# Performance work log

Measured on AMD Instinct MI355X. Metric: run time of the kernel, lower is better.

The kernel has to match this reference:

```python
import jax, jax.numpy as jnp
import numpy as np

K = 3  # conv1d kernel size
PAD = (K - 1) // 2


def _conv1d_1ch(x, w, b):
    # x: (B, 1, C), w: (1, 1, K), b: (1,)  -- torch Conv1d cross-correlation
    c = x.shape[-1]
    xp = jnp.pad(x, ((0, 0), (0, 0), (PAD, PAD)))
    y = sum(w[0, 0, k] * xp[:, :, k:k + c] for k in range(K))
    return y + b[0]


def setup_inputs() -> dict:
    key = jax.random.key(0)
    ks = jax.random.split(key, 13)
    B, C, H, W, E = 8, 256, 48, 48, 64
    s = lambda fan: 1.0 / np.sqrt(fan)
    return {
        "feature": jax.random.normal(ks[0], (B, C, H, W), jnp.float32),
        "wq1": jax.random.normal(ks[1], (1, 1, K), jnp.float32) * s(K),
        "bq1": jax.random.normal(ks[2], (1,), jnp.float32) * s(K),
        "wk1": jax.random.normal(ks[3], (1, 1, K), jnp.float32) * s(K),
        "bk1": jax.random.normal(ks[4], (1,), jnp.float32) * s(K),
        "wq2": jax.random.normal(ks[5], (E, C), jnp.float32) * s(C),
        "bq2": jax.random.normal(ks[6], (E,), jnp.float32) * s(C),
        "wk2": jax.random.normal(ks[7], (E, C), jnp.float32) * s(C),
        "bk2": jax.random.normal(ks[8], (E,), jnp.float32) * s(C),
        "wv2": jax.random.normal(ks[9], (E, C), jnp.float32) * s(C),
        "bv2": jax.random.normal(ks[10], (E,), jnp.float32) * s(C),
        "watt": jax.random.normal(ks[11], (C, E), jnp.float32) * s(E),
        "batt": jax.random.normal(ks[12], (C,), jnp.float32) * s(E),
    }


def reference(feature, wq1, bq1, wk1, bk1, wq2, bq2, wk2, bk2, wv2, bv2, watt, batt):
    b, c, h, w = feature.shape
    hw = h * w

    # ---- Global Channel Attention ----
    gap = jnp.mean(feature, axis=(2, 3)).reshape(b, 1, c)
    query = jax.nn.sigmoid(_conv1d_1ch(gap, wq1, bq1))  # (b,1,c)
    key_ = jax.nn.sigmoid(_conv1d_1ch(gap, wk1, bk1))   # (b,1,c)
    att_c = key_[:, 0, :, None] * query[:, 0, None, :]  # (b,c,c) = K^T Q
    att_c = jax.nn.softmax(att_c, axis=1)               # softmax over dim=1
    value = feature.reshape(b, hw, c)                   # raw reshape, as in torch
    gc = jnp.matmul(value, att_c).reshape(b, c, h, w)   # raw reshape back

    # ---- Global Spatial Attention ----
    q = (jnp.einsum('bchw,ec->behw', feature, wq2) + bq2[None, :, None, None]).reshape(b, -1, hw)
    k = (jnp.einsum('bchw,ec->behw', feature, wk2) + bk2[None, :, None, None]).reshape(b, -1, hw)
    v = (jnp.einsum('bchw,ec->behw', feature, wv2) + bv2[None, :, None, None]).reshape(b, -1, hw)
    att_s = jnp.einsum('bei,bej->bij', k, q)            # (b,hw,hw)
    att_s = jax.nn.softmax(att_s, axis=2)
    gs = jnp.einsum('bei,bij->bej', v, att_s).reshape(b, -1, h, w)  # (b,e,h,w)
    gs = jnp.einsum('behw,ce->bchw', gs, watt) + batt[None, :, None, None]

    # ---- Gated combination ----
    feature_gc = feature * gc
    return feature_gc * gs + feature_gc
```

## Files before the change

kernel.cpp:

```cpp
#include <hip/hip_runtime.h>

#define B_ 8
#define C_ 256
#define HW_ 2304
#define E_ 64
#define SB_ (C_*HW_)
#define LOG2E_ 1.44269504088896340736f

typedef unsigned short u16;
typedef __attribute__((ext_vector_type(8))) __bf16 bf16x8;
typedef __attribute__((ext_vector_type(4))) float f32x4;
#define MFMA16(a,b,c) __builtin_amdgcn_mfma_f32_16x16x32_bf16(a,b,c,0,0,0)

#define LDS_FENCE() do { asm volatile("s_waitcnt lgkmcnt(0)" ::: "memory"); \
                         __builtin_amdgcn_sched_barrier(0); } while(0)

static __device__ inline u16 f2bf(float x){
  unsigned u = __builtin_bit_cast(unsigned, x);
  u += 0x7FFFu + ((u >> 16) & 1u);
  return (u16)(u >> 16);
}
static __device__ inline float bf2f(u16 h){
  unsigned u = ((unsigned)h) << 16;
  return __builtin_bit_cast(float, u);
}


struct KFrag { bf16x8 h0, h1, l0, l1; };
static __device__ __forceinline__ KFrag ldfrag(const u16* __restrict__ ph,
                                               const u16* __restrict__ pl,
                                               size_t tile, int lane){
  KFrag q;
  q.h0 = *(const bf16x8*)(ph + (tile*2+0)*512 + (size_t)lane*8);
  q.h1 = *(const bf16x8*)(ph + (tile*2+1)*512 + (size_t)lane*8);
  q.l0 = *(const bf16x8*)(pl + (tile*2+0)*512 + (size_t)lane*8);
  q.l1 = *(const bf16x8*)(pl + (tile*2+1)*512 + (size_t)lane*8);
  return q;
}

__global__ __launch_bounds__(256) void k_gap(const float* __restrict__ f, float* __restrict__ gap){
  int bc = blockIdx.x;
  const float* row = f + (size_t)bc * HW_;
  float s = 0.f;
  for (int i = threadIdx.x; i < HW_; i += 256) s += row[i];
  #pragma unroll
  for (int off = 32; off; off >>= 1) s += __shfl_down(s, off);
  __shared__ float red[4];
  int lane = threadIdx.x & 63, wv = threadIdx.x >> 6;
  if (lane == 0) red[wv] = s;
  __syncthreads();
  if (threadIdx.x == 0) gap[bc] = (red[0]+red[1]+red[2]+red[3]) * (1.0f/HW_);
}

__global__ __launch_bounds__(256) void k_attc2(const float* __restrict__ gap,
    const float* __restrict__ wq1, const float* __restrict__ bq1,
    const float* __restrict__ wk1, const float* __restrict__ bk1,
    u16* __restrict__ ath, u16* __restrict__ atl){
  int b = blockIdx.x >> 8;
  int j = blockIdx.x & 255;
  int i = threadIdx.x;
  const float* g = gap + b*C_;
  float gm1 = (i > 0)      ? g[i-1] : 0.f;
  float g0  = g[i];
  float gp1 = (i < C_-1)   ? g[i+1] : 0.f;
  float keyv = wk1[0]*gm1 + wk1[1]*g0 + wk1[2]*gp1 + bk1[0];
  keyv = 1.f/(1.f+__expf(-keyv));
  float qm1 = (j > 0)      ? g[j-1] : 0.f;
  float q0  = g[j];
  float qp1 = (j < C_-1)   ? g[j+1] : 0.f;
  float qv = wq1[0]*qm1 + wq1[1]*q0 + wq1[2]*qp1 + bq1[0];
  qv = 1.f/(1.f+__expf(-qv));
  float s = keyv * qv;
  __shared__ float red[256];
  red[i] = s; __syncthreads();
  for (int st = 128; st > 0; st >>= 1){ if (i < st) red[i] = fmaxf(red[i], red[i+st]); __syncthreads(); }
  float mx = red[0]; __syncthreads();
  float e = __expf(s - mx);
  red[i] = e; __syncthreads();
  for (int st = 128; st > 0; st >>= 1){ if (i < st) red[i] += red[i+st]; __syncthreads(); }
  float sum = red[0];
  float x = e / sum;
  u16 hb = f2bf(x);
  size_t o = (((size_t)b*16 + (j>>4))*8 + (i>>5))*512 + (((i&31)>>3)*16 + (j&15))*8 + (i&7);
  ath[o] = hb;
  atl[o] = f2bf(x - bf2f(hb));
}

__global__ __launch_bounds__(256) void k_wcvt(const float* __restrict__ wq,
    const float* __restrict__ wk, const float* __restrict__ wv,
    u16* __restrict__ wbh, u16* __restrict__ wbl){
  int n = blockIdx.x*256 + threadIdx.x;
  int mz = n >> 14; int idx = n & 16383;
  int e = idx >> 8, c = idx & 255;
  const float* w = (mz==0) ? wq : ((mz==1) ? wk : wv);
  float x = w[idx] * ((mz==1) ? LOG2E_ : 1.0f);
  u16 hb = f2bf(x);
  size_t widx = (((size_t)mz*4 + (e>>4))*8 + (c>>5))*512 + (((c&31)>>3)*16 + (e&15))*8 + (c&7);
  wbh[widx] = hb;
  wbl[widx] = f2bf(x - bf2f(hb));
}

__global__ __launch_bounds__(64) void k_proj6(const float* __restrict__ f,
    const u16* __restrict__ wbh, const u16* __restrict__ wbl,
    const float* __restrict__ bq, const float* __restrict__ bk, const float* __restrict__ bv,
    u16* __restrict__ qh, u16* __restrict__ qlo,
    u16* __restrict__ kh, u16* __restrict__ klo,
    u16* __restrict__ vh, u16* __restrict__ vlo){
  int b = blockIdx.x; int p0 = blockIdx.y*16;
  int mz = blockIdx.z >> 1, mh = blockIdx.z & 1;
  int lane = threadIdx.x; int l15 = lane & 15, g = lane >> 4;
  const float* fb = f + (size_t)b*SB_ + p0 + l15;
  const u16* wh = wbh + (size_t)mz*16384;
  const u16* wl = wbl + (size_t)mz*16384;
  const float* bi = (mz==0) ? bq : ((mz==1) ? bk : bv);
  const float bsc = (mz==1) ? LOG2E_ : 1.0f;
  f32x4 c1[2], c2[2], c3[2];
  #pragma unroll
  for (int m = 0; m < 2; m++){
    c1[m] = (f32x4){0.f,0.f,0.f,0.f};
    c2[m] = (f32x4){0.f,0.f,0.f,0.f};
    c3[m] = (f32x4){0.f,0.f,0.f,0.f};
  }
  #pragma unroll
  for (int ks = 0; ks < 8; ks++){
    int cb = ks*32 + g*8;
    float fe[8];
    #pragma unroll
    for (int u = 0; u < 8; u++) fe[u] = fb[(size_t)(cb + u)*HW_];
    union { u16 u[8]; bf16x8 v; } FH, FL;
    #pragma unroll
    for (int u = 0; u < 8; u++){
      u16 hb = f2bf(fe[u]);
      FH.u[u] = hb;
      FL.u[u] = f2bf(fe[u] - bf2f(hb));
    }
    #pragma unroll
    for (int ml = 0; ml < 2; ml++){
      int m = mh*2 + ml;
      bf16x8 awh = *(const bf16x8*)(wh + ((size_t)m*8 + ks)*512 + (size_t)lane*8);
      bf16x8 awl = *(const bf16x8*)(wl + ((size_t)m*8 + ks)*512 + (size_t)lane*8);
      c1[ml] = MFMA16(awh, FH.v, c1[ml]);
      c2[ml] = MFMA16(awh, FL.v, c2[ml]);
      c3[ml] = MFMA16(awl, FH.v, c3[ml]);
    }
  }
  if (mz < 2){
    u16* ohb = (mz==0 ? qh : kh);
    u16* olb = (mz==0 ? qlo: klo);
    size_t tb = ((size_t)b*144 + blockIdx.y)*2;
    #pragma unroll
    for (int ml = 0; ml < 2; ml++){
      int m = mh*2 + ml;
      union { u16 u[4]; uint2 v2; } H, L;
      #pragma unroll
      for (int r = 0; r < 4; r++){
        int e = m*16 + g*4 + r;
        float x = c1[ml][r] + c2[ml][r] + c3[ml][r] + bi[e]*bsc;
        u16 hb = f2bf(x);
        H.u[r] = hb;
        L.u[r] = f2bf(x - bf2f(hb));
      }
      int kc = mh;
      int gc = ml*2 + (g >> 1);
      int ub = (g & 1)*4;
      size_t idx = (tb + kc)*512 + (gc*16 + l15)*8 + ub;
      *(uint2*)(ohb + idx) = H.v2;
      *(uint2*)(olb + idx) = L.v2;
    }
  } else {
    int ic = blockIdx.y >> 1;
    int half = blockIdx.y & 1;
    int gg = half*2 + (l15 >> 3);
    int uu = l15 & 7;
    size_t vb0 = ((size_t)b*72 + ic)*4;
    #pragma unroll
    for (int ml = 0; ml < 2; ml++){
      int m = mh*2 + ml;
      #pragma unroll
      for (int r = 0; r < 4; r++){
        int e = m*16 + g*4 + r;
        float x = c1[ml][r] + c2[ml][r] + c3[ml][r] + bi[e];
        u16 hb = f2bf(x);
        size_t idx = (vb0 + m)*512 + (gg*16 + (g*4 + r))*8 + uu;
        vh[idx] = hb;
        vlo[idx] = f2bf(x - bf2f(hb));
      }
    }
  }
}

__global__ __launch_bounds__(64,2) void k_stats6(
    const u16* __restrict__ qh, const u16* __restrict__ qlo,
    const u16* __restrict__ kh, const u16* __restrict__ klo,
    float* __restrict__ lpart){
  int b = blockIdx.x; int it0 = blockIdx.y; int jz = blockIdx.z;
  int lane = threadIdx.x; int l15 = lane & 15, g = lane >> 4;
  const size_t b144 = (size_t)b*144;
  KFrag kf0 = ldfrag(kh, klo, b144 + it0*2,     lane);
  KFrag kf1 = ldfrag(kh, klo, b144 + it0*2 + 1, lane);
  float lsum[8];
  #pragma unroll
  for (int x = 0; x < 8; x++) lsum[x] = 0.f;
  size_t qb0 = b144 + jz*16;
  #pragma unroll
  for (int t = 0; t < 16; t++){
    KFrag q = ldfrag(qh, qlo, qb0 + t, lane);
    #pragma unroll
    for (int isub = 0; isub < 2; isub++){
      const KFrag& kf = isub ? kf1 : kf0;
      f32x4 c1 = {0.f,0.f,0.f,0.f}, c2 = {0.f,0.f,0.f,0.f}, c3 = {0.f,0.f,0.f,0.f};
      c1 = MFMA16(kf.h0, q.h0, c1);
      c2 = MFMA16(kf.h0, q.l0, c2);
      c3 = MFMA16(kf.l0, q.h0, c3);
      c1 = MFMA16(kf.h1, q.h1, c1);
      c2 = MFMA16(kf.h1, q.l1, c2);
      c3 = MFMA16(kf.l1, q.h1, c3);
      #pragma unroll
      for (int r = 0; r < 4; r++) lsum[isub*4+r] += __builtin_exp2f(c1[r] + c2[r] + c3[r]);
    }
  }
  #pragma unroll
  for (int mk = 1; mk < 16; mk <<= 1){
    #pragma unroll
    for (int x = 0; x < 8; x++) lsum[x] += __shfl_xor(lsum[x], mk);
  }
  if (l15 == 0){
    float* lp = lpart + ((size_t)jz*B_ + b)*HW_ + it0*32;
    #pragma unroll
    for (int isub = 0; isub < 2; isub++)
      #pragma unroll
      for (int r = 0; r < 4; r++) lp[isub*16 + g*4 + r] = lsum[isub*4+r];
  }
}

__global__ __launch_bounds__(256) void k_lrl9(const float* __restrict__ lpart, float* __restrict__ lrl){
  int i = blockIdx.x*256 + threadIdx.x;
  const int BH = B_*HW_;
  float s = 0.f;
  #pragma unroll
  for (int p = 0; p < 9; p++) s += lpart[(size_t)p*BH + i];
  lrl[i] = -__builtin_log2f(s);
}

__global__ __launch_bounds__(64) void k_gs7(
    const u16* __restrict__ qh, const u16* __restrict__ qlo,
    const u16* __restrict__ kh, const u16* __restrict__ klo,
    const u16* __restrict__ vh, const u16* __restrict__ vlo,
    const float* __restrict__ lrl, float* __restrict__ gsp){
  int b = blockIdx.x; int jt0 = blockIdx.y; int iz = blockIdx.z;
  int j0 = jt0*32;
  int lane = threadIdx.x; int l15 = lane & 15, g = lane >> 4;
  __shared__ __align__(16) char smem[10240];
  const size_t b144 = (size_t)b*144;
  KFrag qf0 = ldfrag(qh, qlo, b144 + jt0*2,     lane);
  KFrag qf1 = ldfrag(qh, qlo, b144 + jt0*2 + 1, lane);
  f32x4 gacc[2][4];
  #pragma unroll
  for (int jt = 0; jt < 2; jt++)
    #pragma unroll
    for (int es = 0; es < 4; es++) gacc[jt][es] = (f32x4){0.f,0.f,0.f,0.f};
  const float* lrlb = lrl + b*HW_;
  #pragma unroll 2
  for (int ic = 0; ic < 8; ic++){
    int i0c = iz*256 + ic*32;
    bf16x8 vfh[4], vfl[4];
    size_t vc = ((size_t)b*72 + iz*8 + ic)*4;
    #pragma unroll
    for (int es = 0; es < 4; es++){
      vfh[es] = *(const bf16x8*)(vh  + (vc+es)*512 + (size_t)lane*8);
      vfl[es] = *(const bf16x8*)(vlo + (vc+es)*512 + (size_t)lane*8);
    }
    char* PhB = smem + (ic & 1)*2560;
    char* PlB = smem + 5120 + (ic & 1)*2560;
    #pragma unroll
    for (int msub = 0; msub < 2; msub++){
      KFrag kf = ldfrag(kh, klo, b144 + iz*16 + ic*2 + msub, lane);
      f32x4 rlv = *(const f32x4*)&lrlb[i0c + msub*16 + g*4];
      #pragma unroll
      for (int jt = 0; jt < 2; jt++){
        const KFrag& qf = jt ? qf1 : qf0;
        f32x4 c1 = {0.f,0.f,0.f,0.f}, c2 = {0.f,0.f,0.f,0.f}, c3 = {0.f,0.f,0.f,0.f};
        c1 = MFMA16(kf.h0, qf.h0, c1);
        c2 = MFMA16(kf.h0, qf.l0, c2);
        c3 = MFMA16(kf.l0, qf.h0, c3);
        c1 = MFMA16(kf.h1, qf.h1, c1);
        c2 = MFMA16(kf.h1, qf.l1, c2);
        c3 = MFMA16(kf.l1, qf.h1, c3);
        union { u16 u[4]; uint2 v2; } PH, PL;
        #pragma unroll
        for (int r = 0; r < 4; r++){
          float x = __builtin_exp2f(c1[r] + c2[r] + c3[r] + rlv[r]);
          u16 hb = f2bf(x);
          float hf = bf2f(hb);
          PH.u[r] = hb;
          PL.u[r] = f2bf(x - hf);
        }
        *(uint2*)(PhB + (jt*16 + l15)*80 + msub*32 + g*8) = PH.v2;
        *(uint2*)(PlB + (jt*16 + l15)*80 + msub*32 + g*8) = PL.v2;
      }
    }
    LDS_FENCE();
    #pragma unroll
    for (int jt = 0; jt < 2; jt++){
      bf16x8 pf_h = *(const bf16x8*)(PhB + (jt*16 + l15)*80 + g*16);
      bf16x8 pf_l = *(const bf16x8*)(PlB + (jt*16 + l15)*80 + g*16);
      #pragma unroll
      for (int es = 0; es < 4; es++){
        gacc[jt][es] = MFMA16(vfh[es], pf_h, gacc[jt][es]);
        gacc[jt][es] = MFMA16(vfh[es], pf_l, gacc[jt][es]);
        gacc[jt][es] = MFMA16(vfl[es], pf_h, gacc[jt][es]);
      }
    }
  }
  LDS_FENCE();
  float* GT = (float*)smem;
  #pragma unroll
  for (int jt = 0; jt < 2; jt++)
    #pragma unroll
    for (int es = 0; es < 4; es++)
      #pragma unroll
      for (int r = 0; r < 4; r++)
        GT[(es*16 + g*4 + r)*32 + jt*16 + l15] = gacc[jt][es][r];
  LDS_FENCE();
  float* gb = gsp + ((size_t)iz*B_ + b)*E_*HW_;
  #pragma unroll
  for (int itx = 0; itx < 8; itx++){
    int n = (itx*64 + lane)*4;
    f32x4 vv = *(const f32x4*)&GT[n];
    int e = n >> 5, jj = n & 31;
    *(f32x4*)&gb[(size_t)e*HW_ + j0 + jj] = vv;
  }
}

__global__ __launch_bounds__(256) void k_gsum9(const float* __restrict__ gsp, float* __restrict__ gs){
  const size_t N = (size_t)B_*E_*HW_;
  size_t n = ((size_t)blockIdx.x*256 + threadIdx.x)*4;
  f32x4 s = *(const f32x4*)(gsp + n);
  #pragma unroll
  for (int p = 1; p < 9; p++) s += *(const f32x4*)(gsp + (size_t)p*N + n);
  *(f32x4*)(gs + n) = s;
}

__global__ __launch_bounds__(256) void k_gsout2(const float* __restrict__ gs,
    const float* __restrict__ watt, const float* __restrict__ batt,
    float* __restrict__ gsout){
  int b = blockIdx.x; int sc = blockIdx.y; int cc0 = blockIdx.z * 16;
  int s = sc*256 + threadIdx.x;
  const float* gb = gs + (size_t)b*E_*HW_ + s;
  float acc[16];
  #pragma unroll
  for (int x = 0; x < 16; x++) acc[x] = 0.f;
  for (int e = 0; e < E_; e++){
    float gv = gb[(size_t)e*HW_];
    #pragma unroll
    for (int x = 0; x < 16; x++) acc[x] += watt[(cc0+x)*E_ + e] * gv;
  }
  float* ob = gsout + (size_t)b*SB_ + (size_t)cc0*HW_ + s;
  #pragma unroll
  for (int x = 0; x < 16; x++) ob[(size_t)x*HW_] = acc[x] + batt[cc0 + x];
}

__global__ __launch_bounds__(64) void k_final3(const float* __restrict__ f,
    const u16* __restrict__ ath, const u16* __restrict__ atl,
    float* __restrict__ inout){
  int b = blockIdx.x; int s0 = blockIdx.y*16; int z = blockIdx.z;
  int lane = threadIdx.x; int l15 = lane & 15, g = lane >> 4;
  const float* fb = f + (size_t)b*SB_;
  bf16x8 Ah[8], Al[8];
  const float* arow = fb + (size_t)(s0 + l15)*C_;
  #pragma unroll
  for (int ks = 0; ks < 8; ks++){
    int cbase = ks*32 + g*8;
    float4 f4a = *(const float4*)&arow[cbase];
    float4 f4b = *(const float4*)&arow[cbase + 4];
    float fe[8] = {f4a.x, f4a.y, f4a.z, f4a.w, f4b.x, f4b.y, f4b.z, f4b.w};
    union { u16 u[8]; bf16x8 v; } H, L;
    #pragma unroll
    for (int e = 0; e < 8; e++){
      u16 hb = f2bf(fe[e]);
      H.u[e] = hb;
      L.u[e] = f2bf(fe[e] - bf2f(hb));
    }
    Ah[ks] = H.v; Al[ks] = L.v;
  }
  const u16* abz_h = ath + (size_t)b*65536;
  const u16* abz_l = atl + (size_t)b*65536;
  f32x4 acc[4];
  #pragma unroll
  for (int q = 0; q < 4; q++) acc[q] = (f32x4){0.f,0.f,0.f,0.f};
  #pragma unroll
  for (int q = 0; q < 4; q++){
    int jt = z*4 + q;
    #pragma unroll
    for (int ks = 0; ks < 8; ks++){
      bf16x8 Bh = *(const bf16x8*)(abz_h + ((size_t)jt*8 + ks)*512 + (size_t)lane*8);
      bf16x8 Bl = *(const bf16x8*)(abz_l + ((size_t)jt*8 + ks)*512 + (size_t)lane*8);
      acc[q] = MFMA16(Ah[ks], Bh, acc[q]);
      acc[q] = MFMA16(Ah[ks], Bl, acc[q]);
      acc[q] = MFMA16(Al[ks], Bh, acc[q]);
    }
  }
  float* ob = inout + (size_t)b*SB_;
  #pragma unroll
  for (int q = 0; q < 4; q++){
    #pragma unroll
    for (int r = 0; r < 4; r++){
      int p = s0 + g*4 + r;
      int j = (z*4+q)*16 + l15;
      size_t n = (size_t)p*C_ + j;
      float fx = fb[n];
      float gso = ob[n];
      ob[n] = acc[q][r] * fx * (gso + 1.f);
    }
  }
}

extern "C" void kernel_launch(void* const* d_in, const int* in_sizes, int n_in,
                              void* d_out, int out_size, void* d_ws, size_t ws_size,
                              hipStream_t stream){
  const float* f    = (const float*)d_in[0];
  const float* wq1  = (const float*)d_in[1];
  const float* bq1  = (const float*)d_in[2];
  const float* wk1  = (const float*)d_in[3];
  const float* bk1  = (const float*)d_in[4];
  const float* wq2  = (const float*)d_in[5];
  const float* bq2  = (const float*)d_in[6];
  const float* wk2  = (const float*)d_in[7];
  const float* bk2  = (const float*)d_in[8];
  const float* wv2  = (const float*)d_in[9];
  const float* bv2  = (const float*)d_in[10];
  const float* watt = (const float*)d_in[11];
  const float* batt = (const float*)d_in[12];
  float* out = (float*)d_out;
  char* W = (char*)d_ws;

  float* gap   = (float*)(W + 0);
  u16*   ath   = (u16*)  (W + 8192);
  u16*   atl   = (u16*)  (W + 1056768);
  float* lpart = (float*)(W + 2105344);
  float* lrl   = (float*)(W + 2768896);
  float* gsp   = (float*)(W + 2842624);
  float* gs    = (float*)(W + 45309952);
  u16* qh  = (u16*)(W + 50028544);
  u16* qlo = (u16*)(W + 52387840);
  u16* kh  = (u16*)(W + 54747136);
  u16* klo = (u16*)(W + 57106432);
  u16* vh  = (u16*)(W + 59465728);
  u16* vlo = (u16*)(W + 61825024);
  u16* wbh = (u16*)(W + 64184320);
  u16* wbl = (u16*)(W + 64282624);

  k_gap   <<<B_*C_,             256, 0, stream>>>(f, gap);
  k_attc2 <<<B_*C_,             256, 0, stream>>>(gap, wq1, bq1, wk1, bk1, ath, atl);
  k_wcvt  <<<192,               256, 0, stream>>>(wq2, wk2, wv2, wbh, wbl);
  k_proj6 <<<dim3(B_, 144, 6),   64, 0, stream>>>(f, wbh, wbl, bq2, bk2, bv2,
                                                  qh, qlo, kh, klo, vh, vlo);
  k_stats6<<<dim3(B_, 72, 9),    64, 0, stream>>>(qh, qlo, kh, klo, lpart);
  k_lrl9  <<<B_*HW_/256,        256, 0, stream>>>(lpart, lrl);
  k_gs7   <<<dim3(B_, 72, 9),    64, 0, stream>>>(qh, qlo, kh, klo, vh, vlo, lrl, gsp);
  k_gsum9 <<<B_*E_*HW_/1024,    256, 0, stream>>>(gsp, gs);
  k_gsout2<<<dim3(B_, 9, 16),   256, 0, stream>>>(gs, watt, batt, out);
  k_final3<<<dim3(B_, 144, 4),   64, 0, stream>>>(f, ath, atl, out);
}
```

Measured before the change: 165.3 us.

## Fold softmax normalization into V, use wave-shuffle reductions, widen gsout tiles

Stops adding a per-row log-normaliser inside the exp of the spatial attention kernel. A new pass instead rescales the V hi/lo split values by the reciprocal row sum before the P·V product, so k_gs no longer loads lrl. The channel-attention softmax replaces its LDS tree reductions with wave shuffles plus one small cross-wave step. k_gsout now computes 32 output channels per block instead of 16, and k_gs gets a min-waves occupancy hint. The changes add an extra kernel launch and a read-modify-write of V, and unnormalised exp values may lose some bf16 precision.

```diff
diff --git a/kernel.cpp b/kernel.cpp
--- a/kernel.cpp
+++ b/kernel.cpp
@@ -52,7 +52,7 @@
   if (threadIdx.x == 0) gap[bc] = (red[0]+red[1]+red[2]+red[3]) * (1.0f/HW_);
 }
 
-__global__ __launch_bounds__(256) void k_attc2(const float* __restrict__ gap,
+__global__ __launch_bounds__(256) void k_attc3(const float* __restrict__ gap,
     const float* __restrict__ wq1, const float* __restrict__ bq1,
     const float* __restrict__ wk1, const float* __restrict__ bk1,
     u16* __restrict__ ath, u16* __restrict__ atl){
@@ -71,14 +71,21 @@
   float qv = wq1[0]*qm1 + wq1[1]*q0 + wq1[2]*qp1 + bq1[0];
   qv = 1.f/(1.f+__expf(-qv));
   float s = keyv * qv;
-  __shared__ float red[256];
-  red[i] = s; __syncthreads();
-  for (int st = 128; st > 0; st >>= 1){ if (i < st) red[i] = fmaxf(red[i], red[i+st]); __syncthreads(); }
-  float mx = red[0]; __syncthreads();
+  __shared__ float red[8];
+  int wv = i >> 6, ln = i & 63;
+  float m = s;
+  #pragma unroll
+  for (int off = 32; off; off >>= 1) m = fmaxf(m, __shfl_xor(m, off));
+  if (ln == 0) red[wv] = m;
+  __syncthreads();
+  float mx = fmaxf(fmaxf(red[0], red[1]), fmaxf(red[2], red[3]));
   float e = __expf(s - mx);
-  red[i] = e; __syncthreads();
-  for (int st = 128; st > 0; st >>= 1){ if (i < st) red[i] += red[i+st]; __syncthreads(); }
-  float sum = red[0];
+  float sm = e;
+  #pragma unroll
+  for (int off = 32; off; off >>= 1) sm += __shfl_xor(sm, off);
+  if (ln == 0) red[4 + wv] = sm;
+  __syncthreads();
+  float sum = (red[4] + red[5]) + (red[6] + red[7]);
   float x = e / sum;
   u16 hb = f2bf(x);
   size_t o = (((size_t)b*16 + (j>>4))*8 + (i>>5))*512 + (((i&31)>>3)*16 + (j&15))*8 + (i&7);
@@ -233,20 +240,50 @@
   }
 }
 
-__global__ __launch_bounds__(256) void k_lrl9(const float* __restrict__ lpart, float* __restrict__ lrl){
+__global__ __launch_bounds__(256) void k_rli9(const float* __restrict__ lpart, float* __restrict__ rl){
   int i = blockIdx.x*256 + threadIdx.x;
   const int BH = B_*HW_;
   float s = 0.f;
   #pragma unroll
   for (int p = 0; p < 9; p++) s += lpart[(size_t)p*BH + i];
-  lrl[i] = -__builtin_log2f(s);
-}
-
-__global__ __launch_bounds__(64) void k_gs7(
+  rl[i] = 1.0f / s;
+}
+
+__global__ __launch_bounds__(256) void k_vscale(const float* __restrict__ rl,
+    u16* __restrict__ vh, u16* __restrict__ vlo){
+  int flat = blockIdx.x*256 + threadIdx.x;
+  int lane = flat & 63;
+  int slot = flat >> 6;
+  int b = slot / 288;
+  int rem = slot - b*288;
+  int ic = rem >> 2;
+  int g = lane >> 4;
+  const float* rb = rl + b*HW_ + ic*32 + g*8;
+  f32x4 r0 = *(const f32x4*)rb;
+  f32x4 r1 = *(const f32x4*)(rb + 4);
+  u16* ph = vh  + (size_t)slot*512 + (size_t)lane*8;
+  u16* pl = vlo + (size_t)slot*512 + (size_t)lane*8;
+  union { u16 u[8]; uint4 v; } H, L;
+  H.v = *(const uint4*)ph;
+  L.v = *(const uint4*)pl;
+  #pragma unroll
+  for (int u = 0; u < 8; u++){
+    float v = bf2f(H.u[u]) + bf2f(L.u[u]);
+    float r = (u < 4) ? r0[u] : r1[u-4];
+    float x = v * r;
+    u16 hb = f2bf(x);
+    H.u[u] = hb;
+    L.u[u] = f2bf(x - bf2f(hb));
+  }
+  *(uint4*)ph = H.v;
+  *(uint4*)pl = L.v;
+}
+
+__global__ __launch_bounds__(64,5) void k_gs11(
     const u16* __restrict__ qh, const u16* __restrict__ qlo,
     const u16* __restrict__ kh, const u16* __restrict__ klo,
     const u16* __restrict__ vh, const u16* __restrict__ vlo,
-    const float* __restrict__ lrl, float* __restrict__ gsp){
+    float* __restrict__ gsp){
   int b = blockIdx.x; int jt0 = blockIdx.y; int iz = blockIdx.z;
   int j0 = jt0*32;
   int lane = threadIdx.x; int l15 = lane & 15, g = lane >> 4;
@@ -259,10 +296,8 @@
   for (int jt = 0; jt < 2; jt++)
     #pragma unroll
     for (int es = 0; es < 4; es++) gacc[jt][es] = (f32x4){0.f,0.f,0.f,0.f};
-  const float* lrlb = lrl + b*HW_;
   #pragma unroll 2
   for (int ic = 0; ic < 8; ic++){
-    int i0c = iz*256 + ic*32;
     bf16x8 vfh[4], vfl[4];
     size_t vc = ((size_t)b*72 + iz*8 + ic)*4;
     #pragma unroll
@@ -275,7 +310,6 @@
     #pragma unroll
     for (int msub = 0; msub < 2; msub++){
       KFrag kf = ldfrag(kh, klo, b144 + iz*16 + ic*2 + msub, lane);
-      f32x4 rlv = *(const f32x4*)&lrlb[i0c + msub*16 + g*4];
       #pragma unroll
       for (int jt = 0; jt < 2; jt++){
         const KFrag& qf = jt ? qf1 : qf0;
@@ -289,7 +323,7 @@
         union { u16 u[4]; uint2 v2; } PH, PL;
         #pragma unroll
         for (int r = 0; r < 4; r++){
-          float x = __builtin_exp2f(c1[r] + c2[r] + c3[r] + rlv[r]);
+          float x = __builtin_exp2f(c1[r] + c2[r] + c3[r]);
           u16 hb = f2bf(x);
           float hf = bf2f(hb);
           PH.u[r] = hb;
@@ -341,23 +375,23 @@
   *(f32x4*)(gs + n) = s;
 }
 
-__global__ __launch_bounds__(256) void k_gsout2(const float* __restrict__ gs,
+__global__ __launch_bounds__(256) void k_gsout3(const float* __restrict__ gs,
     const float* __restrict__ watt, const float* __restrict__ batt,
     float* __restrict__ gsout){
-  int b = blockIdx.x; int sc = blockIdx.y; int cc0 = blockIdx.z * 16;
+  int b = blockIdx.x; int sc = blockIdx.y; int cc0 = blockIdx.z * 32;
   int s = sc*256 + threadIdx.x;
   const float* gb = gs + (size_t)b*E_*HW_ + s;
-  float acc[16];
-  #pragma unroll
-  for (int x = 0; x < 16; x++) acc[x] = 0.f;
+  float acc[32];
+  #pragma unroll
+  for (int x = 0; x < 32; x++) acc[x] = 0.f;
   for (int e = 0; e < E_; e++){
     float gv = gb[(size_t)e*HW_];
     #pragma unroll
-    for (int x = 0; x < 16; x++) acc[x] += watt[(cc0+x)*E_ + e] * gv;
+    for (int x = 0; x < 32; x++) acc[x] += watt[(cc0+x)*E_ + e] * gv;
   }
   float* ob = gsout + (size_t)b*SB_ + (size_t)cc0*HW_ + s;
   #pragma unroll
-  for (int x = 0; x < 16; x++) ob[(size_t)x*HW_] = acc[x] + batt[cc0 + x];
+  for (int x = 0; x < 32; x++) ob[(size_t)x*HW_] = acc[x] + batt[cc0 + x];
 }
 
 __global__ __launch_bounds__(64) void k_final3(const float* __restrict__ f,
@@ -438,7 +472,7 @@
   u16*   ath   = (u16*)  (W + 8192);
   u16*   atl   = (u16*)  (W + 1056768);
   float* lpart = (float*)(W + 2105344);
-  float* lrl   = (float*)(W + 2768896);
+  float* rl    = (float*)(W + 2768896);
   float* gsp   = (float*)(W + 2842624);
   float* gs    = (float*)(W + 45309952);
   u16* qh  = (u16*)(W + 50028544);
@@ -451,14 +485,15 @@
   u16* wbl = (u16*)(W + 64282624);
 
   k_gap   <<<B_*C_,             256, 0, stream>>>(f, gap);
-  k_attc2 <<<B_*C_,             256, 0, stream>>>(gap, wq1, bq1, wk1, bk1, ath, atl);
+  k_attc3 <<<B_*C_,             256, 0, stream>>>(gap, wq1, bq1, wk1, bk1, ath, atl);
   k_wcvt  <<<192,               256, 0, stream>>>(wq2, wk2, wv2, wbh, wbl);
   k_proj6 <<<dim3(B_, 144, 6),   64, 0, stream>>>(f, wbh, wbl, bq2, bk2, bv2,
                                                   qh, qlo, kh, klo, vh, vlo);
   k_stats6<<<dim3(B_, 72, 9),    64, 0, stream>>>(qh, qlo, kh, klo, lpart);
-  k_lrl9  <<<B_*HW_/256,        256, 0, stream>>>(lpart, lrl);
-  k_gs7   <<<dim3(B_, 72, 9),    64, 0, stream>>>(qh, qlo, kh, klo, vh, vlo, lrl, gsp);
+  k_rli9  <<<B_*HW_/256,        256, 0, stream>>>(lpart, rl);
+  k_vscale<<<576,               256, 0, stream>>>(rl, vh, vlo);
+  k_gs11  <<<dim3(B_, 72, 9),    64, 0, stream>>>(qh, qlo, kh, klo, vh, vlo, gsp);
   k_gsum9 <<<B_*E_*HW_/1024,    256, 0, stream>>>(gsp, gs);
-  k_gsout2<<<dim3(B_, 9, 16),   256, 0, stream>>>(gs, watt, batt, out);
+  k_gsout3<<<dim3(B_, 9, 8),    256, 0, stream>>>(gs, watt, batt, out);
   k_final3<<<dim3(B_, 144, 4),   64, 0, stream>>>(f, ath, atl, out);
 }
```

New measurement: 169.4 us. 1.02x slower.
